# Optimization experiments

Measured on AMD Instinct MI355X. Metric: run time of the kernel, lower is better.

The kernel has to match this reference:

```python
import jax, jax.numpy as jnp
import numpy as np

B, S = 16, 1024
D_MODEL, N_MEL = 256, 80
IN_DIM = D_MODEL * (((N_MEL - 1) // 2 - 1) // 2)  # 4864
G, V, CV_DIM = 2, 320, 256


def setup_inputs() -> dict:
    key = jax.random.key(0)
    k1, k2, k3 = jax.random.split(key, 3)
    hidden_states = jax.random.normal(k1, (B, S, IN_DIM), dtype=jnp.float32)
    W = jax.random.normal(k2, (IN_DIM, G * V), dtype=jnp.float32) / np.sqrt(IN_DIM)
    b = jnp.zeros((G * V,), dtype=jnp.float32)
    codevectors = jax.random.normal(k3, (1, G * V, CV_DIM // G), dtype=jnp.float32)
    return {"hidden_states": hidden_states, "W": W, "b": b,
            "codevectors": codevectors, "num_groups": G}


def reference(hidden_states, W, b, codevectors, num_groups):
    bsz, seq, _ = hidden_states.shape
    logits = hidden_states @ W + b                      # (B, S, G*V)
    gv = logits.shape[-1]
    nvars = gv // num_groups
    flat = logits.reshape(bsz * seq, num_groups, nvars)  # (BS, G, V)
    idx = jnp.argmax(flat, axis=-1)                      # (BS, G) int
    # one-hot codevector probs (eval / hard argmax branch)
    probs = jax.nn.one_hot(idx, nvars, dtype=logits.dtype)  # (BS, G, V)
    marginal = probs.mean(axis=0)                        # (G, V)
    perplexity = jnp.exp(-jnp.sum(marginal * jnp.log(marginal + 1e-7), axis=-1)).sum()
    # weighted sum over codebook == gather of selected codevector per group
    cv = codevectors.reshape(num_groups, nvars, -1)      # (G, V, Dg)
    gathered = cv[jnp.arange(num_groups)[None, :], idx]  # (BS, G, Dg)
    out = gathered.reshape(bsz, seq, -1)                 # (B, S, codevector_dim)
    return (out, perplexity)
```

## Files before the change

kernel.cpp:

```cpp
#include <hip/hip_runtime.h>
#include <stdint.h>

#define M_TOT 16384
#define K_TOT 4864
#define N_TOT 640
#define GRP   2
#define NV    320
#define CVD   128

#define BM 128
#define BN 320
#define BK 32
#define KITERS (K_TOT / BK)

#define MARGIN 5.0e-4f

typedef __attribute__((ext_vector_type(8))) short short8;
typedef __attribute__((ext_vector_type(4))) float f32x4;

#define WS_FLAGCNT  0
#define WS_COUNTS   256
#define WS_FLAGLIST 4096
#define FLAGCAP     32768
#define WS_PACKED   (4096 + 262144)
#define WS_WT       (1u << 20)

__device__ __forceinline__ unsigned int mono_u32(float f) {
    unsigned int b = __float_as_uint(f);
    return b ^ ((unsigned int)((int)b >> 31) | 0x80000000u);
}
__device__ __forceinline__ unsigned short f2bf(float x) {
    unsigned int u = __float_as_uint(x);
    return (unsigned short)((u + 0x7fffu + ((u >> 16) & 1u)) >> 16);
}
__device__ __forceinline__ float bf2f(unsigned short h) {
    return __uint_as_float(((unsigned int)h) << 16);
}
__device__ __forceinline__ void gld16(const void* g, void* l) {
    __builtin_amdgcn_global_load_lds(
        (const __attribute__((address_space(1))) unsigned int*)g,
        (__attribute__((address_space(3))) unsigned int*)l, 16, 0, 0);
}

__global__ __launch_bounds__(256)
void convert_wt(const float* __restrict__ W, unsigned short* __restrict__ wt)
{
    __shared__ float sW[64][68];
    const int k0 = blockIdx.x * 64;
    const int n0 = blockIdx.y * 64;
    const int tid = threadIdx.x;
    for (int l = tid; l < 64 * 16; l += 256) {
        int kr = l >> 4, nc = (l & 15) * 4;
        float4 v = *(const float4*)(W + (size_t)(k0 + kr) * N_TOT + n0 + nc);
        sW[kr][nc] = v.x; sW[kr][nc + 1] = v.y; sW[kr][nc + 2] = v.z; sW[kr][nc + 3] = v.w;
    }
    __syncthreads();
    unsigned short* whi = wt;
    unsigned short* wlo = wt + (size_t)N_TOT * K_TOT;
    for (int l = tid; l < 64 * 8; l += 256) {
        int nr = l >> 3, ko = (l & 7) * 8;
        union { short8 v; unsigned short u[8]; } hu, lu;
#pragma unroll
        for (int j = 0; j < 8; ++j) {
            float x = sW[ko + j][nr];
            unsigned short hb = f2bf(x);
            hu.u[j] = hb;
            lu.u[j] = f2bf(x - bf2f(hb));
        }
        size_t off = (size_t)(n0 + nr) * K_TOT + k0 + ko;
        *(short8*)(whi + off) = hu.v;
        *(short8*)(wlo + off) = lu.v;
    }
}

__device__ __forceinline__ void stage_b(const unsigned short* __restrict__ wt,
                                        short* sBbuf, int bx, int kk, int tid)
{
#pragma unroll
    for (int r = 0; r < 5; ++r) {
        int c = r * 512 + tid;
        int row = c >> 3, slot = c & 7;
        int sv = slot ^ (row & 7);
        int half = sv >> 2, oct = sv & 3;
        const unsigned short* gp = wt + (size_t)half * N_TOT * K_TOT
            + (size_t)(bx * NV + row) * K_TOT + kk + (oct << 3);
        gld16(gp, sBbuf + (size_t)c * 8);
    }
}

__global__ __launch_bounds__(512, 2)
void gemm_mfma(const float* __restrict__ A, const unsigned short* __restrict__ wt,
               const float* __restrict__ bias,
               unsigned long long* __restrict__ packed,
               unsigned int* __restrict__ flagcnt, unsigned int* __restrict__ flaglist)
{
    __shared__ short sA[2][BM][64];
    __shared__ short sB[2][BN][64];
    __shared__ uint4 sRed[BM][4];

    const int tid  = threadIdx.x;
    const int L    = tid & 63;
    const int w    = tid >> 6;
    const int quad = L >> 4;
    const int lrow = L & 15;
    const int wrow = w >> 2;
    const int wcol = w & 3;
    const int bx   = blockIdx.x;
    const int m0   = blockIdx.y * BM;

    const int sh = (quad ^ (lrow & 7)) << 3;
    const int sl = ((4 | quad) ^ (lrow & 7)) << 3;

    const int arow = tid >> 2;
    const int aoct = tid & 3;
    const float* Ap = A + (size_t)(m0 + arow) * K_TOT + aoct * 8;
    const int sHa = (aoct ^ (arow & 7)) << 3;
    const int sLa = ((4 | aoct) ^ (arow & 7)) << 3;

    f32x4 acc[4][5];
#pragma unroll
    for (int i = 0; i < 4; ++i)
#pragma unroll
        for (int j = 0; j < 5; ++j) acc[i][j] = (f32x4){0.f, 0.f, 0.f, 0.f};

    {
        float4 a0 = *(const float4*)(Ap);
        float4 a1 = *(const float4*)(Ap + 4);
        stage_b(wt, &sB[0][0][0], bx, 0, tid);
        union { short8 v; unsigned short u[8]; } hu, lu;
        float xs[8] = {a0.x, a0.y, a0.z, a0.w, a1.x, a1.y, a1.z, a1.w};
#pragma unroll
        for (int j = 0; j < 8; ++j) {
            unsigned short hb = f2bf(xs[j]);
            hu.u[j] = hb; lu.u[j] = f2bf(xs[j] - bf2f(hb));
        }
        *(short8*)&sA[0][arow][sHa] = hu.v;
        *(short8*)&sA[0][arow][sLa] = lu.v;
    }
    __syncthreads();

    int k0 = 0;
    for (int it = 0; it < KITERS; ++it) {
        const int buf = it & 1;
        const int kn  = k0 + BK;
        float4 a0, a1;
        const bool more = (it + 1 < KITERS);
        if (more) {
            a0 = *(const float4*)(Ap + kn);
            a1 = *(const float4*)(Ap + kn + 4);
            stage_b(wt, &sB[buf ^ 1][0][0], bx, kn, tid);
        }
        short8 ah[4], al[4];
#pragma unroll
        for (int fi = 0; fi < 4; ++fi) {
            int mloc = wrow * 64 + fi * 16 + lrow;
            ah[fi] = *(const short8*)&sA[buf][mloc][sh];
            al[fi] = *(const short8*)&sA[buf][mloc][sl];
        }
#pragma unroll
        for (int fj = 0; fj < 5; ++fj) {
            int nloc = wcol * 80 + fj * 16 + lrow;
            short8 bh = *(const short8*)&sB[buf][nloc][sh];
            short8 bl = *(const short8*)&sB[buf][nloc][sl];
#pragma unroll
            for (int fi = 0; fi < 4; ++fi) {
                acc[fi][fj] = __builtin_amdgcn_mfma_f32_16x16x32_bf16(ah[fi], bh, acc[fi][fj], 0, 0, 0);
                acc[fi][fj] = __builtin_amdgcn_mfma_f32_16x16x32_bf16(ah[fi], bl, acc[fi][fj], 0, 0, 0);
                acc[fi][fj] = __builtin_amdgcn_mfma_f32_16x16x32_bf16(al[fi], bh, acc[fi][fj], 0, 0, 0);
            }
        }
        if (more) {
            union { short8 v; unsigned short u[8]; } hu, lu;
            float xs[8] = {a0.x, a0.y, a0.z, a0.w, a1.x, a1.y, a1.z, a1.w};
#pragma unroll
            for (int j = 0; j < 8; ++j) {
                unsigned short hb = f2bf(xs[j]);
                hu.u[j] = hb; lu.u[j] = f2bf(xs[j] - bf2f(hb));
            }
            *(short8*)&sA[buf ^ 1][arow][sHa] = hu.v;
            *(short8*)&sA[buf ^ 1][arow][sLa] = lu.v;
        }
        __syncthreads();
        k0 = kn;
    }

    float bs[5];
#pragma unroll
    for (int fj = 0; fj < 5; ++fj)
        bs[fj] = bias[bx * NV + wcol * 80 + fj * 16 + lrow];

#pragma unroll
    for (int fi = 0; fi < 4; ++fi) {
#pragma unroll
        for (int r = 0; r < 4; ++r) {
            unsigned long long pv = 0; float v1 = 0.f, v2 = -3.4e38f;
#pragma unroll
            for (int fj = 0; fj < 5; ++fj) {
                float v = acc[fi][fj][r] + bs[fj];
                int cig = wcol * 80 + fj * 16 + lrow;
                unsigned long long p = ((unsigned long long)mono_u32(v) << 32)
                                     | (unsigned int)(NV - 1 - cig);
                if (fj == 0) { pv = p; v1 = v; }
                else if (p > pv) { v2 = v1; v1 = v; pv = p; }
                else { v2 = fmaxf(v2, v); }
            }
#pragma unroll
            for (int msk = 1; msk < 16; msk <<= 1) {
                unsigned long long opv = __shfl_xor(pv, msk);
                float ov1 = __shfl_xor(v1, msk);
                float ov2 = __shfl_xor(v2, msk);
                if (opv > pv) { v2 = fmaxf(v1, ov2); v1 = ov1; pv = opv; }
                else          { v2 = fmaxf(v2, ov1); }
            }
            if (lrow == 0) {
                int row_blk = wrow * 64 + fi * 16 + quad * 4 + r;
                uint4 e;
                e.x = (unsigned int)(pv & 0xFFFFFFFFull);
                e.y = (unsigned int)(pv >> 32);
                e.z = __float_as_uint(v2);
                e.w = __float_as_uint(v1);
                sRed[row_blk][wcol] = e;
            }
        }
    }
    __syncthreads();

    if (tid < BM) {
        unsigned long long pv = 0; float v1 = -3.4e38f, v2 = -3.4e38f;
#pragma unroll
        for (int wc = 0; wc < 4; ++wc) {
            uint4 e = sRed[tid][wc];
            unsigned long long opv = ((unsigned long long)e.y << 32) | e.x;
            float ov1 = __uint_as_float(e.w), ov2 = __uint_as_float(e.z);
            if (opv > pv) { v2 = fmaxf(v1, ov2); v1 = ov1; pv = opv; }
            else          { v2 = fmaxf(v2, ov1); }
        }
        packed[(size_t)(m0 + tid) * GRP + bx] = pv;
        if (v1 - v2 <= MARGIN) {
            unsigned int slot = atomicAdd(&flagcnt[bx], 1u);
            flaglist[bx * FLAGCAP + slot] = (unsigned int)(m0 + tid);
        }
    }
}

#define RCH_IPB 4
__global__ __launch_bounds__(320)
void recheck(const float* __restrict__ A, const float* __restrict__ W,
             const float* __restrict__ bias,
             const unsigned int* __restrict__ flagcnt,
             const unsigned int* __restrict__ flaglist,
             unsigned long long* __restrict__ packed)
{
    __shared__ float  sAr[RCH_IPB][K_TOT];
    __shared__ float4 sPart[RCH_IPB][320];
    __shared__ float  sVals[RCH_IPB][NV];
    __shared__ int    sRow[RCH_IPB];
    const int tid = threadIdx.x;
    const int g   = blockIdx.x & 1;
    const unsigned int cnt = flagcnt[g];
    const unsigned int* list = flaglist + g * FLAGCAP;
    const int kseg = tid / 80, c4 = tid % 80;
    for (unsigned int base = (unsigned int)(blockIdx.x >> 1) * RCH_IPB; base < cnt;
         base += (unsigned int)(gridDim.x >> 1) * RCH_IPB) {
        const unsigned int nit = (cnt - base < (unsigned int)RCH_IPB)
                               ? (cnt - base) : (unsigned int)RCH_IPB;
        __syncthreads();
        if (tid < RCH_IPB) {
            unsigned int src = base + (unsigned int)tid;
            if (src >= cnt) src = base;
            sRow[tid] = (int)list[src];
        }
        __syncthreads();
        for (int l = tid; l < RCH_IPB * (K_TOT / 4); l += 320) {
            int j = l / (K_TOT / 4), off = l - j * (K_TOT / 4);
            *(float4*)&sAr[j][off * 4] =
                *(const float4*)(A + (size_t)sRow[j] * K_TOT + off * 4);
        }
        __syncthreads();
        float4 ac0 = {0.f,0.f,0.f,0.f}, ac1 = {0.f,0.f,0.f,0.f};
        float4 ac2 = {0.f,0.f,0.f,0.f}, ac3 = {0.f,0.f,0.f,0.f};
        const float* wp = W + (size_t)(kseg * 1216) * N_TOT + g * NV + c4 * 4;
        const float* a0p = &sAr[0][kseg * 1216];
        const float* a1p = &sAr[1][kseg * 1216];
        const float* a2p = &sAr[2][kseg * 1216];
        const float* a3p = &sAr[3][kseg * 1216];
        for (int k = 0; k < 1216; ++k) {
            float4 wv = *(const float4*)(wp + (size_t)k * N_TOT);
            float av0 = a0p[k], av1 = a1p[k], av2 = a2p[k], av3 = a3p[k];
            ac0.x = fmaf(av0, wv.x, ac0.x); ac0.y = fmaf(av0, wv.y, ac0.y);
            ac0.z = fmaf(av0, wv.z, ac0.z); ac0.w = fmaf(av0, wv.w, ac0.w);
            ac1.x = fmaf(av1, wv.x, ac1.x); ac1.y = fmaf(av1, wv.y, ac1.y);
            ac1.z = fmaf(av1, wv.z, ac1.z); ac1.w = fmaf(av1, wv.w, ac1.w);
            ac2.x = fmaf(av2, wv.x, ac2.x); ac2.y = fmaf(av2, wv.y, ac2.y);
            ac2.z = fmaf(av2, wv.z, ac2.z); ac2.w = fmaf(av2, wv.w, ac2.w);
            ac3.x = fmaf(av3, wv.x, ac3.x); ac3.y = fmaf(av3, wv.y, ac3.y);
            ac3.z = fmaf(av3, wv.z, ac3.z); ac3.w = fmaf(av3, wv.w, ac3.w);
        }
        sPart[0][tid] = ac0; sPart[1][tid] = ac1;
        sPart[2][tid] = ac2; sPart[3][tid] = ac3;
        __syncthreads();
        if (tid < 80) {
#pragma unroll
            for (int j = 0; j < RCH_IPB; ++j) {
                float4 s = {0.f, 0.f, 0.f, 0.f};
#pragma unroll
                for (int ks = 0; ks < 4; ++ks) {
                    float4 p = sPart[j][ks * 80 + tid];
                    s.x += p.x; s.y += p.y; s.z += p.z; s.w += p.w;
                }
                float4 bb = *(const float4*)(bias + g * NV + tid * 4);
                sVals[j][tid * 4 + 0] = s.x + bb.x;
                sVals[j][tid * 4 + 1] = s.y + bb.y;
                sVals[j][tid * 4 + 2] = s.z + bb.z;
                sVals[j][tid * 4 + 3] = s.w + bb.w;
            }
        }
        __syncthreads();
        if (tid < (int)nit) {
            float best = sVals[tid][0]; int bi = 0;
            for (int c = 1; c < NV; ++c)
                if (sVals[tid][c] > best) { best = sVals[tid][c]; bi = c; }
            packed[(size_t)sRow[tid] * GRP + g] =
                ((unsigned long long)mono_u32(best) << 32) | (unsigned int)(NV - 1 - bi);
        }
    }
}

__global__ __launch_bounds__(256)
void gather_hist(const unsigned long long* __restrict__ packed,
                 const float* __restrict__ cv,
                 float* __restrict__ out, int* __restrict__ counts)
{
    const int t = threadIdx.x;
    const int g = t >> 7;
    const int c = t & 127;
    for (int m = blockIdx.x; m < M_TOT; m += gridDim.x) {
        const unsigned long long p = packed[(size_t)m * GRP + g];
        const int idx = (NV - 1) - (int)(p & 0xFFFFFFFFull);
        out[(size_t)m * (GRP * CVD) + t] = cv[((size_t)g * NV + idx) * CVD + c];
        if (c == 0) atomicAdd(&counts[g * NV + idx], 1);
    }
}

__global__ void perplexity_k(const int* __restrict__ counts, float* __restrict__ outp)
{
    __shared__ float sred[GRP * NV];
    const int t = threadIdx.x;
    const float marg = (float)counts[t] * (1.0f / (float)M_TOT);
    sred[t] = marg * logf(marg + 1e-7f);
    __syncthreads();
    if (t < GRP) {
        float s = 0.f;
        for (int i = 0; i < NV; ++i) s += sred[t * NV + i];
        sred[t] = expf(-s);
    }
    __syncthreads();
    if (t == 0) outp[0] = sred[0] + sred[1];
}

extern "C" void kernel_launch(void* const* d_in, const int* in_sizes, int n_in,
                              void* d_out, int out_size, void* d_ws, size_t ws_size,
                              hipStream_t stream)
{
    const float* A    = (const float*)d_in[0];
    const float* Wm   = (const float*)d_in[1];
    const float* bias = (const float*)d_in[2];
    const float* cv   = (const float*)d_in[3];

    float* out = (float*)d_out;
    float* ppl = out + (size_t)M_TOT * (GRP * CVD);

    char* ws = (char*)d_ws;
    unsigned int*       flagcnt  = (unsigned int*)(ws + WS_FLAGCNT);
    int*                counts   = (int*)(ws + WS_COUNTS);
    unsigned int*       flaglist = (unsigned int*)(ws + WS_FLAGLIST);
    unsigned long long* packed   = (unsigned long long*)(ws + WS_PACKED);
    unsigned short*     wt       = (unsigned short*)(ws + WS_WT);

    hipMemsetAsync(d_ws, 0, 4096, stream);
    convert_wt<<<dim3(76, 10), 256, 0, stream>>>(Wm, wt);
    gemm_mfma<<<dim3(2, 128), 512, 0, stream>>>(A, wt, bias, packed, flagcnt, flaglist);
    recheck<<<256, 320, 0, stream>>>(A, Wm, bias, flagcnt, flaglist, packed);
    gather_hist<<<4096, 256, 0, stream>>>(packed, cv, out, counts);
    perplexity_k<<<1, GRP * NV, 0, stream>>>(counts, ppl);
}
```

Measured before the change: 881.1 us.

## Fuse gather and histogram into GEMM epilogue; recheck only near-max candidate columns

The GEMM epilogue now writes the selected codevector rows to the output and accumulates the histogram counts directly, which removes the separate gather_hist kernel. It also records, for each flagged near-tie row, only the columns within the margin of the max as candidates. Recheck then recomputes those few columns exactly in fp32 and fixes packed, counts and output only when the winner changes, instead of recomputing all 320 logits per flagged row. The cost is that each recheck block linearly scans the whole candidate list, and a candidate buffer overflow would silently drop candidates.

```diff
diff --git a/kernel.cpp b/kernel.cpp
--- a/kernel.cpp
+++ b/kernel.cpp
@@ -19,10 +19,13 @@
 typedef __attribute__((ext_vector_type(4))) float f32x4;
 
 #define WS_FLAGCNT  0
+#define WS_CANDCNT  4
 #define WS_COUNTS   256
 #define WS_FLAGLIST 4096
 #define FLAGCAP     32768
-#define WS_PACKED   (4096 + 262144)
+#define WS_CANDLIST (4096 + 131072)
+#define CANDCAP     65536
+#define WS_PACKED   (512 * 1024)
 #define WS_WT       (1u << 20)
 
 __device__ __forceinline__ unsigned int mono_u32(float f) {
@@ -90,13 +93,17 @@
 
 __global__ __launch_bounds__(512, 2)
 void gemm_mfma(const float* __restrict__ A, const unsigned short* __restrict__ wt,
-               const float* __restrict__ bias,
+               const float* __restrict__ bias, const float* __restrict__ cv,
+               float* __restrict__ out, int* __restrict__ counts,
                unsigned long long* __restrict__ packed,
-               unsigned int* __restrict__ flagcnt, unsigned int* __restrict__ flaglist)
+               unsigned int* __restrict__ flagcnt, unsigned int* __restrict__ flaglist,
+               unsigned int* __restrict__ candcnt, unsigned int* __restrict__ candlist)
 {
     __shared__ short sA[2][BM][64];
     __shared__ short sB[2][BN][64];
     __shared__ uint4 sRed[BM][4];
+    __shared__ float sThr[BM];
+    __shared__ unsigned sWin[BM];
 
     const int tid  = threadIdx.x;
     const int L    = tid & 63;
@@ -236,109 +243,111 @@
             else          { v2 = fmaxf(v2, ov1); }
         }
         packed[(size_t)(m0 + tid) * GRP + bx] = pv;
-        if (v1 - v2 <= MARGIN) {
-            unsigned int slot = atomicAdd(&flagcnt[bx], 1u);
-            flaglist[bx * FLAGCAP + slot] = (unsigned int)(m0 + tid);
-        }
-    }
-}
-
-#define RCH_IPB 4
-__global__ __launch_bounds__(320)
+        unsigned widx = (NV - 1) - (unsigned)(pv & 0xFFFFFFFFull);
+        sWin[tid] = widx;
+        atomicAdd(&counts[bx * NV + widx], 1);
+        bool fl = (v1 - v2 <= MARGIN);
+        sThr[tid] = fl ? (v1 - MARGIN) : 3.4e38f;
+        if (fl) {
+            unsigned int slot = atomicAdd(flagcnt, 1u);
+            flaglist[slot] = ((unsigned int)(m0 + tid) << 1) | (unsigned int)bx;
+        }
+    }
+    __syncthreads();
+
+#pragma unroll
+    for (int fi = 0; fi < 4; ++fi) {
+#pragma unroll
+        for (int r = 0; r < 4; ++r) {
+            int row_blk = wrow * 64 + fi * 16 + quad * 4 + r;
+            float thr = sThr[row_blk];
+            if (thr < 1.0e38f) {
+#pragma unroll
+                for (int fj = 0; fj < 5; ++fj) {
+                    float v = acc[fi][fj][r] + bs[fj];
+                    if (v >= thr) {
+                        int cig = wcol * 80 + fj * 16 + lrow;
+                        unsigned int slot = atomicAdd(candcnt, 1u);
+                        if (slot < CANDCAP)
+                            candlist[slot] = ((unsigned int)(m0 + row_blk) << 10)
+                                           | ((unsigned int)bx << 9) | (unsigned int)cig;
+                    }
+                }
+            }
+        }
+    }
+
+    {
+        int row = tid >> 2, q = tid & 3;
+        unsigned idx = sWin[row];
+        const float4* cvp = (const float4*)(cv + ((size_t)bx * NV + idx) * CVD + q * 32);
+        float4* op = (float4*)(out + (size_t)(m0 + row) * (GRP * CVD) + bx * CVD + q * 32);
+#pragma unroll
+        for (int j = 0; j < 8; ++j) op[j] = cvp[j];
+    }
+}
+
+__global__ __launch_bounds__(256)
 void recheck(const float* __restrict__ A, const float* __restrict__ W,
-             const float* __restrict__ bias,
+             const float* __restrict__ bias, const float* __restrict__ cv,
              const unsigned int* __restrict__ flagcnt,
              const unsigned int* __restrict__ flaglist,
-             unsigned long long* __restrict__ packed)
-{
-    __shared__ float  sAr[RCH_IPB][K_TOT];
-    __shared__ float4 sPart[RCH_IPB][320];
-    __shared__ float  sVals[RCH_IPB][NV];
-    __shared__ int    sRow[RCH_IPB];
+             const unsigned int* __restrict__ candcnt,
+             const unsigned int* __restrict__ candlist,
+             unsigned long long* __restrict__ packed,
+             float* __restrict__ out, int* __restrict__ counts)
+{
+    __shared__ float sPart[256];
+    __shared__ unsigned long long sBest;
+    __shared__ unsigned sOld, sNew;
     const int tid = threadIdx.x;
-    const int g   = blockIdx.x & 1;
-    const unsigned int cnt = flagcnt[g];
-    const unsigned int* list = flaglist + g * FLAGCAP;
-    const int kseg = tid / 80, c4 = tid % 80;
-    for (unsigned int base = (unsigned int)(blockIdx.x >> 1) * RCH_IPB; base < cnt;
-         base += (unsigned int)(gridDim.x >> 1) * RCH_IPB) {
-        const unsigned int nit = (cnt - base < (unsigned int)RCH_IPB)
-                               ? (cnt - base) : (unsigned int)RCH_IPB;
+    const unsigned fcnt = *flagcnt;
+    unsigned ccnt = *candcnt; if (ccnt > CANDCAP) ccnt = CANDCAP;
+    for (unsigned i = blockIdx.x; i < fcnt; i += gridDim.x) {
+        unsigned item = flaglist[i];
+        int m = (int)(item >> 1), g = (int)(item & 1);
+        const unsigned key = item;
+        const float* ap = A + (size_t)m * K_TOT;
+        if (tid == 0) sBest = 0ull;
         __syncthreads();
-        if (tid < RCH_IPB) {
-            unsigned int src = base + (unsigned int)tid;
-            if (src >= cnt) src = base;
-            sRow[tid] = (int)list[src];
+        for (unsigned j = 0; j < ccnt; ++j) {
+            unsigned e = candlist[j];
+            if ((e >> 9) != key) continue;
+            int c = (int)(e & 511);
+            const float* wp = W + (size_t)tid * N_TOT + g * NV + c;
+            float part = 0.f;
+#pragma unroll
+            for (int jj = 0; jj < 19; ++jj)
+                part = fmaf(ap[tid + 256 * jj], wp[(size_t)jj * 256 * N_TOT], part);
+            sPart[tid] = part;
+            __syncthreads();
+            for (int s = 128; s > 0; s >>= 1) {
+                if (tid < s) sPart[tid] += sPart[tid + s];
+                __syncthreads();
+            }
+            if (tid == 0) {
+                float val = sPart[0] + bias[g * NV + c];
+                unsigned long long pk = ((unsigned long long)mono_u32(val) << 32)
+                                      | (unsigned int)(NV - 1 - c);
+                if (pk > sBest) sBest = pk;
+            }
+            __syncthreads();
+        }
+        if (tid == 0) {
+            unsigned long long oldp = packed[(size_t)m * GRP + g];
+            sOld = (NV - 1) - (unsigned)(oldp & 0xFFFFFFFFull);
+            sNew = (NV - 1) - (unsigned)(sBest & 0xFFFFFFFFull);
+            if (sBest != oldp) packed[(size_t)m * GRP + g] = sBest;
+            if (sNew != sOld) {
+                atomicSub((unsigned int*)&counts[g * NV + sOld], 1u);
+                atomicAdd(&counts[g * NV + sNew], 1);
+            }
         }
         __syncthreads();
-        for (int l = tid; l < RCH_IPB * (K_TOT / 4); l += 320) {
-            int j = l / (K_TOT / 4), off = l - j * (K_TOT / 4);
-            *(float4*)&sAr[j][off * 4] =
-                *(const float4*)(A + (size_t)sRow[j] * K_TOT + off * 4);
-        }
+        if (sNew != sOld && tid < CVD)
+            out[(size_t)m * (GRP * CVD) + g * CVD + tid] =
+                cv[((size_t)g * NV + sNew) * CVD + tid];
         __syncthreads();
-        float4 ac0 = {0.f,0.f,0.f,0.f}, ac1 = {0.f,0.f,0.f,0.f};
-        float4 ac2 = {0.f,0.f,0.f,0.f}, ac3 = {0.f,0.f,0.f,0.f};
-        const float* wp = W + (size_t)(kseg * 1216) * N_TOT + g * NV + c4 * 4;
-        const float* a0p = &sAr[0][kseg * 1216];
-        const float* a1p = &sAr[1][kseg * 1216];
-        const float* a2p = &sAr[2][kseg * 1216];
-        const float* a3p = &sAr[3][kseg * 1216];
-        for (int k = 0; k < 1216; ++k) {
-            float4 wv = *(const float4*)(wp + (size_t)k * N_TOT);
-            float av0 = a0p[k], av1 = a1p[k], av2 = a2p[k], av3 = a3p[k];
-            ac0.x = fmaf(av0, wv.x, ac0.x); ac0.y = fmaf(av0, wv.y, ac0.y);
-            ac0.z = fmaf(av0, wv.z, ac0.z); ac0.w = fmaf(av0, wv.w, ac0.w);
-            ac1.x = fmaf(av1, wv.x, ac1.x); ac1.y = fmaf(av1, wv.y, ac1.y);
-            ac1.z = fmaf(av1, wv.z, ac1.z); ac1.w = fmaf(av1, wv.w, ac1.w);
-            ac2.x = fmaf(av2, wv.x, ac2.x); ac2.y = fmaf(av2, wv.y, ac2.y);
-            ac2.z = fmaf(av2, wv.z, ac2.z); ac2.w = fmaf(av2, wv.w, ac2.w);
-            ac3.x = fmaf(av3, wv.x, ac3.x); ac3.y = fmaf(av3, wv.y, ac3.y);
-            ac3.z = fmaf(av3, wv.z, ac3.z); ac3.w = fmaf(av3, wv.w, ac3.w);
-        }
-        sPart[0][tid] = ac0; sPart[1][tid] = ac1;
-        sPart[2][tid] = ac2; sPart[3][tid] = ac3;
-        __syncthreads();
-        if (tid < 80) {
-#pragma unroll
-            for (int j = 0; j < RCH_IPB; ++j) {
-                float4 s = {0.f, 0.f, 0.f, 0.f};
-#pragma unroll
-                for (int ks = 0; ks < 4; ++ks) {
-                    float4 p = sPart[j][ks * 80 + tid];
-                    s.x += p.x; s.y += p.y; s.z += p.z; s.w += p.w;
-                }
-                float4 bb = *(const float4*)(bias + g * NV + tid * 4);
-                sVals[j][tid * 4 + 0] = s.x + bb.x;
-                sVals[j][tid * 4 + 1] = s.y + bb.y;
-                sVals[j][tid * 4 + 2] = s.z + bb.z;
-                sVals[j][tid * 4 + 3] = s.w + bb.w;
-            }
-        }
-        __syncthreads();
-        if (tid < (int)nit) {
-            float best = sVals[tid][0]; int bi = 0;
-            for (int c = 1; c < NV; ++c)
-                if (sVals[tid][c] > best) { best = sVals[tid][c]; bi = c; }
-            packed[(size_t)sRow[tid] * GRP + g] =
-                ((unsigned long long)mono_u32(best) << 32) | (unsigned int)(NV - 1 - bi);
-        }
-    }
-}
-
-__global__ __launch_bounds__(256)
-void gather_hist(const unsigned long long* __restrict__ packed,
-                 const float* __restrict__ cv,
-                 float* __restrict__ out, int* __restrict__ counts)
-{
-    const int t = threadIdx.x;
-    const int g = t >> 7;
-    const int c = t & 127;
-    for (int m = blockIdx.x; m < M_TOT; m += gridDim.x) {
-        const unsigned long long p = packed[(size_t)m * GRP + g];
-        const int idx = (NV - 1) - (int)(p & 0xFFFFFFFFull);
-        out[(size_t)m * (GRP * CVD) + t] = cv[((size_t)g * NV + idx) * CVD + c];
-        if (c == 0) atomicAdd(&counts[g * NV + idx], 1);
     }
 }
 
@@ -372,15 +381,19 @@
 
     char* ws = (char*)d_ws;
     unsigned int*       flagcnt  = (unsigned int*)(ws + WS_FLAGCNT);
+    unsigned int*       candcnt  = (unsigned int*)(ws + WS_CANDCNT);
     int*                counts   = (int*)(ws + WS_COUNTS);
     unsigned int*       flaglist = (unsigned int*)(ws + WS_FLAGLIST);
+    unsigned int*       candlist = (unsigned int*)(ws + WS_CANDLIST);
     unsigned long long* packed   = (unsigned long long*)(ws + WS_PACKED);
     unsigned short*     wt       = (unsigned short*)(ws + WS_WT);
 
     hipMemsetAsync(d_ws, 0, 4096, stream);
     convert_wt<<<dim3(76, 10), 256, 0, stream>>>(Wm, wt);
-    gemm_mfma<<<dim3(2, 128), 512, 0, stream>>>(A, wt, bias, packed, flagcnt, flaglist);
-    recheck<<<256, 320, 0, stream>>>(A, Wm, bias, flagcnt, flaglist, packed);
-    gather_hist<<<4096, 256, 0, stream>>>(packed, cv, out, counts);
+    gemm_mfma<<<dim3(2, 128), 512, 0, stream>>>(A, wt, bias, cv, out, counts,
+                                                packed, flagcnt, flaglist,
+                                                candcnt, candlist);
+    recheck<<<512, 256, 0, stream>>>(A, Wm, bias, cv, flagcnt, flaglist,
+                                     candcnt, candlist, packed, out, counts);
     perplexity_k<<<1, GRP * NV, 0, stream>>>(counts, ppl);
 }
```

Result: faster. 723.4 us (-17.9%).
